# Performance work log

Measured on AMD Instinct MI355X. Metric: run time of the kernel, lower is better.

Reference implementation:

```python
import jax, jax.numpy as jnp
import numpy as np

B, L, N, DOUT = 8, 8192, 256, 256  # batch, seq_len, state_dim, output_dim


def setup_inputs() -> dict:
    key = jax.random.key(0)
    k_u, k_h, k_w = jax.random.split(key, 3)
    u = jax.random.normal(k_u, (B, L, 1), dtype=jnp.float32)
    # impulse response buffer (stands in for A_bar^i @ B_bar rows); decay-scaled for realism
    h = jax.random.normal(k_h, (L, N), dtype=jnp.float32) * 0.02
    W = jax.random.normal(k_w, (DOUT, N), dtype=jnp.float32) * (1.0 / np.sqrt(N))
    return {"u": u, "h": h, "W": W}


def reference(u, h, W):
    L_ = h.shape[0]
    n_fft = 2 * L_
    # FFT-based long convolution: U:[B, n_fft//2+1, 1], H:[n_fft//2+1, N]
    U = jnp.fft.rfft(u, n=n_fft, axis=1)
    H = jnp.fft.rfft(h, n=n_fft, axis=0)
    M = U * H[None, :, :]                      # broadcast channel 1 -> N
    m = jnp.fft.irfft(M, n=n_fft, axis=1)[:, :L_, :]  # [B, L, N]
    return jnp.einsum('bln,on->blo', m, W)     # Linear(state_dim -> output_dim), no bias
```

## Files before the change

kernel.cpp:

```cpp
#include <hip/hip_runtime.h>
#include <hip/hip_bf16.h>
#include <stdint.h>
#include <stddef.h>

typedef __attribute__((ext_vector_type(4))) float f32x4;
typedef __attribute__((ext_vector_type(8))) short s16x8;

#define B_    8
#define L_    8192
#define N_    256
#define DOUT_ 256

__device__ __forceinline__ unsigned short f2bf(float f) {
  unsigned int x = __float_as_uint(f);
  x += 0x7fff + ((x >> 16) & 1);
  return (unsigned short)(x >> 16);
}

__global__ void k_convert(const float* __restrict__ h, const float* __restrict__ W,
                          unsigned short* __restrict__ hb, unsigned short* __restrict__ Wb) {
  int t = blockIdx.x * 256 + threadIdx.x;
  int base = t * 4;
  const int TH = L_ * N_;
  const int TW = DOUT_ * N_;
  if (base < TH) {
    float4 v = *(const float4*)(h + base);
    hb[base + 0] = f2bf(v.x); hb[base + 1] = f2bf(v.y);
    hb[base + 2] = f2bf(v.z); hb[base + 3] = f2bf(v.w);
  } else if (base < TH + TW) {
    int wb = base - TH;
    float4 v = *(const float4*)(W + wb);
    Wb[wb + 0] = f2bf(v.x); Wb[wb + 1] = f2bf(v.y);
    Wb[wb + 2] = f2bf(v.z); Wb[wb + 3] = f2bf(v.w);
  }
}

__global__ void k_amat(const float* __restrict__ u, unsigned short* __restrict__ Am) {
  int t = blockIdx.x * 256 + threadIdx.x;
  int i0 = (t & 15) * 8;
  int lp = (t >> 4) & 127;
  int d  = (t >> 11) & 63;
  int b  = t >> 17;
  const float* ub = u + b * L_;
  int base = 128 * d + lp - i0;
  s16x8 v;
#pragma unroll
  for (int j = 0; j < 8; ++j) {
    int idx = base - j;
    float f = (idx >= 0) ? ub[idx] : 0.0f;
    v[j] = (short)f2bf(f);
  }
  *(s16x8*)(Am + (size_t)t * 8) = v;
}

__global__ void k_gt(const unsigned short* __restrict__ Wb, const unsigned short* __restrict__ hb,
                     unsigned short* __restrict__ gT) {
  int gid  = blockIdx.x * 256 + threadIdx.x;
  int lane = gid & 63;
  int wid  = gid >> 6;
  int o_t  = wid >> 7;
  int i_t  = wid & 127;
  int o0 = o_t * 16, i0 = i_t * 64;
  int ln = lane & 15, hi = lane >> 4;
  f32x4 acc[4] = {};
#pragma unroll
  for (int k0 = 0; k0 < N_; k0 += 32) {
    s16x8 a = *(const s16x8*)(Wb + (o0 + ln) * N_ + k0 + 8 * hi);
#pragma unroll
    for (int ns = 0; ns < 4; ++ns) {
      s16x8 bfr = *(const s16x8*)(hb + (i0 + 16 * ns + ln) * N_ + k0 + 8 * hi);
      acc[ns] = __builtin_amdgcn_mfma_f32_16x16x32_bf16(a, bfr, acc[ns], 0, 0, 0);
    }
  }
#pragma unroll
  for (int ns = 0; ns < 4; ++ns)
#pragma unroll
    for (int q = 0; q < 4; ++q)
      gT[(size_t)(o0 + 4 * hi + q) * L_ + i0 + 16 * ns + ln] = f2bf(acc[ns][q]);
}

__global__ __launch_bounds__(256) void k_main(const unsigned short* __restrict__ Am,
                                              const unsigned short* __restrict__ gT,
                                              float* __restrict__ out) {
  __shared__ short Abuf[128 * 64];
  __shared__ short Bbuf[128 * 64];
  const int c = blockIdx.x;
  const int b = blockIdx.y;
  const int r = 63 - blockIdx.z;
  const int t = threadIdx.x;
  const int lane = t & 63;
  const int w = t >> 6;
  const int wm = (w >> 1) * 64, wn = (w & 1) * 64;
  const int ln = lane & 15, hi = lane >> 4;
  const int ob = c * 128;
  const int trow = t >> 3;
  const int tcol = (t & 7) * 8;
  f32x4 acc[4][4] = {};

  const int nkt = 2 * (r + 1);
  for (int kt = 0; kt < nkt; ++kt) {
    const int i0   = kt * 64;
    const int d    = r - (kt >> 1);
    const int ioff = (kt & 1) * 64;
    const unsigned short* Asrc = Am + (((size_t)(b * 64 + d)) << 14) + ioff + tcol;
    const unsigned short* Bsrc = gT + (size_t)(ob + trow) * L_ + i0 + tcol;
#pragma unroll
    for (int call = 0; call < 4; ++call) {
      __builtin_amdgcn_global_load_lds(
          (const __attribute__((address_space(1))) void*)(Asrc + (size_t)(call * 32 + trow) * 128),
          (__attribute__((address_space(3))) void*)(Abuf + call * 2048 + t * 8),
          16, 0, 0);
    }
#pragma unroll
    for (int call = 0; call < 4; ++call) {
      __builtin_amdgcn_global_load_lds(
          (const __attribute__((address_space(1))) void*)(Bsrc + (size_t)(call * 32) * L_),
          (__attribute__((address_space(3))) void*)(Bbuf + call * 2048 + t * 8),
          16, 0, 0);
    }
    __syncthreads();
#pragma unroll
    for (int k0 = 0; k0 < 64; k0 += 32) {
      s16x8 af[4], bfr[4];
#pragma unroll
      for (int m = 0; m < 4; ++m)
        af[m] = *(const s16x8*)(Abuf + (wm + m * 16 + ln) * 64 + k0 + 8 * hi);
#pragma unroll
      for (int n = 0; n < 4; ++n)
        bfr[n] = *(const s16x8*)(Bbuf + (wn + n * 16 + ln) * 64 + k0 + 8 * hi);
#pragma unroll
      for (int m = 0; m < 4; ++m)
#pragma unroll
        for (int n = 0; n < 4; ++n)
          acc[m][n] = __builtin_amdgcn_mfma_f32_16x16x32_bf16(af[m], bfr[n], acc[m][n], 0, 0, 0);
    }
    __syncthreads();
  }

  const int lb = r * 128;
#pragma unroll
  for (int m = 0; m < 4; ++m)
#pragma unroll
    for (int n = 0; n < 4; ++n)
#pragma unroll
      for (int q = 0; q < 4; ++q) {
        int l = lb + wm + m * 16 + 4 * hi + q;
        int o = ob + wn + n * 16 + ln;
        out[(size_t)(b * L_ + l) * DOUT_ + o] = acc[m][n][q];
      }
}

extern "C" void kernel_launch(void* const* d_in, const int* in_sizes, int n_in,
                              void* d_out, int out_size, void* d_ws, size_t ws_size,
                              hipStream_t stream) {
  const float* u = (const float*)d_in[0];
  const float* h = (const float*)d_in[1];
  const float* W = (const float*)d_in[2];
  float* out = (float*)d_out;

  char* ws = (char*)d_ws;
  unsigned short* hb = (unsigned short*)(ws);
  unsigned short* Wb = (unsigned short*)(ws + (size_t)4 * 1024 * 1024);
  unsigned short* gT = (unsigned short*)(ws + (size_t)4 * 1024 * 1024 + 131072);
  unsigned short* Am = (unsigned short*)(ws + (size_t)8 * 1024 * 1024 + 131072);

  k_convert<<<2112, 256, 0, stream>>>(h, W, hb, Wb);
  k_amat<<<4096, 256, 0, stream>>>(u, Am);
  k_gt<<<512, 256, 0, stream>>>(Wb, hb, gT);
  k_main<<<dim3(2, 8, 64), 256, 0, stream>>>(Am, gT, out);
}
```

Before: 220.4 us.

## Double-buffer main GEMM with 256-row tiles, LDS swizzle and zero block padding

Restructures the main Toeplitz-GEMM kernel to use 512-thread blocks with 256-row output tiles and double-buffered LDS filled by async global-to-LDS loads that overlap the MFMA compute. LDS reads use an XOR swizzle to avoid bank conflicts, and MFMA sections run at raised wave priority. A zero diagonal block (index 64) is added to the A matrix so tiles reaching before the sequence start read zeros instead of branching. hb now aliases the Am workspace region, so k_amat is reordered to run after k_gt. The costs are more LDS per block, fewer total blocks, and extra causal work on the padded zero blocks.

```diff
diff --git a/kernel.cpp b/kernel.cpp
--- a/kernel.cpp
+++ b/kernel.cpp
@@ -39,16 +39,21 @@
   int t = blockIdx.x * 256 + threadIdx.x;
   int i0 = (t & 15) * 8;
   int lp = (t >> 4) & 127;
-  int d  = (t >> 11) & 63;
-  int b  = t >> 17;
-  const float* ub = u + b * L_;
-  int base = 128 * d + lp - i0;
+  int r2 = t >> 11;
+  int d  = r2 % 65;
+  int b  = r2 / 65;
   s16x8 v;
 #pragma unroll
-  for (int j = 0; j < 8; ++j) {
-    int idx = base - j;
-    float f = (idx >= 0) ? ub[idx] : 0.0f;
-    v[j] = (short)f2bf(f);
+  for (int j = 0; j < 8; ++j) v[j] = 0;
+  if (d < 64) {
+    const float* ub = u + b * L_;
+    int base = 128 * d + lp - i0;
+#pragma unroll
+    for (int j = 0; j < 8; ++j) {
+      int idx = base - j;
+      float f = (idx >= 0) ? ub[idx] : 0.0f;
+      v[j] = (short)f2bf(f);
+    }
   }
   *(s16x8*)(Am + (size_t)t * 8) = v;
 }
@@ -79,75 +84,131 @@
       gT[(size_t)(o0 + 4 * hi + q) * L_ + i0 + 16 * ns + ln] = f2bf(acc[ns][q]);
 }
 
-__global__ __launch_bounds__(256) void k_main(const unsigned short* __restrict__ Am,
-                                              const unsigned short* __restrict__ gT,
-                                              float* __restrict__ out) {
-  __shared__ short Abuf[128 * 64];
-  __shared__ short Bbuf[128 * 64];
+__global__ __launch_bounds__(512, 2) void k_main(const unsigned short* __restrict__ Am,
+                                                 const unsigned short* __restrict__ gT,
+                                                 float* __restrict__ out) {
+  __shared__ short As[2][16384];
+  __shared__ short Bs[2][8192];
   const int c = blockIdx.x;
   const int b = blockIdx.y;
-  const int r = 63 - blockIdx.z;
-  const int t = threadIdx.x;
-  const int lane = t & 63;
-  const int w = t >> 6;
-  const int wm = (w >> 1) * 64, wn = (w & 1) * 64;
+  const int R = 31 - blockIdx.z;
+  const int tid = threadIdx.x;
+  const int lane = tid & 63;
+  const int w = tid >> 6;
+  const int wr = w >> 1, wc = w & 1;
   const int ln = lane & 15, hi = lane >> 4;
   const int ob = c * 128;
-  const int trow = t >> 3;
-  const int tcol = (t & 7) * 8;
+
+  const int t3 = tid >> 3;
+  const int sA = ((tid & 7) ^ (t3 & 7)) << 3;
+  const unsigned short* AmB = Am + (size_t)(b * 65) * 16384;
+  const unsigned short* Bb0 = gT + (size_t)(ob + t3) * L_ + sA;
+  const unsigned short* Bb1 = gT + (size_t)(ob + t3 + 64) * L_ + sA;
+  const int rl0 = t3;
+  const int rl1 = 64 + t3;
+
+  const int offA = (wr * 64 + ln) * 64;
+  const int offB = (wc * 64 + ln) * 64;
+  const int sw = ln & 7;
+  const int off_k0 = (hi ^ sw) * 8;
+  const int off_k1 = ((hi + 4) ^ sw) * 8;
+
   f32x4 acc[4][4] = {};
-
-  const int nkt = 2 * (r + 1);
+  const int nkt = 4 * (R + 1);
+
+#define ISSUE_A(ktv, buf) do { \
+    const int kthalf_ = (ktv) >> 1; const int kodd_ = ((ktv) & 1) << 6; \
+    _Pragma("unroll") \
+    for (int q = 0; q < 4; ++q) { \
+      int dd = 2 * R + (q >> 1) - kthalf_; \
+      int sd = dd < 0 ? 64 : dd; \
+      const unsigned short* src = AmB + ((size_t)sd << 14) + ((q & 1 ? rl1 : rl0) << 7) + kodd_ + sA; \
+      __builtin_amdgcn_global_load_lds((const __attribute__((address_space(1))) void*)src, \
+          (__attribute__((address_space(3))) void*)(&As[buf][(tid + 512 * q) * 8]), 16, 0, 0); \
+    } \
+  } while (0)
+
+#define ISSUE_B(ktv, buf) do { \
+    const int kb_ = (ktv) * 64; \
+    __builtin_amdgcn_global_load_lds((const __attribute__((address_space(1))) void*)(Bb0 + kb_), \
+        (__attribute__((address_space(3))) void*)(&Bs[buf][tid * 8]), 16, 0, 0); \
+    __builtin_amdgcn_global_load_lds((const __attribute__((address_space(1))) void*)(Bb1 + kb_), \
+        (__attribute__((address_space(3))) void*)(&Bs[buf][(tid + 512) * 8]), 16, 0, 0); \
+  } while (0)
+
+  ISSUE_A(0, 0);
+  ISSUE_B(0, 0);
+
   for (int kt = 0; kt < nkt; ++kt) {
-    const int i0   = kt * 64;
-    const int d    = r - (kt >> 1);
-    const int ioff = (kt & 1) * 64;
-    const unsigned short* Asrc = Am + (((size_t)(b * 64 + d)) << 14) + ioff + tcol;
-    const unsigned short* Bsrc = gT + (size_t)(ob + trow) * L_ + i0 + tcol;
-#pragma unroll
-    for (int call = 0; call < 4; ++call) {
-      __builtin_amdgcn_global_load_lds(
-          (const __attribute__((address_space(1))) void*)(Asrc + (size_t)(call * 32 + trow) * 128),
-          (__attribute__((address_space(3))) void*)(Abuf + call * 2048 + t * 8),
-          16, 0, 0);
-    }
-#pragma unroll
-    for (int call = 0; call < 4; ++call) {
-      __builtin_amdgcn_global_load_lds(
-          (const __attribute__((address_space(1))) void*)(Bsrc + (size_t)(call * 32) * L_),
-          (__attribute__((address_space(3))) void*)(Bbuf + call * 2048 + t * 8),
-          16, 0, 0);
-    }
-    __syncthreads();
-#pragma unroll
-    for (int k0 = 0; k0 < 64; k0 += 32) {
-      s16x8 af[4], bfr[4];
+    const int cur = kt & 1;
+    const int nxt = cur ^ 1;
+    const int kt1 = (kt + 1 < nkt) ? kt + 1 : kt;
+
+    ISSUE_A(kt1, nxt);
+    asm volatile("s_waitcnt vmcnt(4)" ::: "memory");
+    __builtin_amdgcn_sched_barrier(0);
+    __builtin_amdgcn_s_barrier();
+    __builtin_amdgcn_sched_barrier(0);
+    const short* Ac = &As[cur][0];
+    const short* Bc = &Bs[cur][0];
+    s16x8 af[4][2], bf[2][2];
+#pragma unroll
+    for (int m = 0; m < 4; ++m) {
+      af[m][0] = *(const s16x8*)(Ac + offA + m * 1024 + off_k0);
+      af[m][1] = *(const s16x8*)(Ac + offA + m * 1024 + off_k1);
+    }
+#pragma unroll
+    for (int n = 0; n < 2; ++n) {
+      bf[n][0] = *(const s16x8*)(Bc + offB + n * 1024 + off_k0);
+      bf[n][1] = *(const s16x8*)(Bc + offB + n * 1024 + off_k1);
+    }
+    __builtin_amdgcn_s_setprio(1);
+#pragma unroll
+    for (int kk = 0; kk < 2; ++kk)
 #pragma unroll
       for (int m = 0; m < 4; ++m)
-        af[m] = *(const s16x8*)(Abuf + (wm + m * 16 + ln) * 64 + k0 + 8 * hi);
+#pragma unroll
+        for (int n = 0; n < 2; ++n)
+          acc[m][n] = __builtin_amdgcn_mfma_f32_16x16x32_bf16(af[m][kk], bf[n][kk], acc[m][n], 0, 0, 0);
+    __builtin_amdgcn_s_setprio(0);
+
+    ISSUE_B(kt1, nxt);
+    s16x8 bg[2][2];
+#pragma unroll
+    for (int n = 0; n < 2; ++n) {
+      bg[n][0] = *(const s16x8*)(Bc + offB + (n + 2) * 1024 + off_k0);
+      bg[n][1] = *(const s16x8*)(Bc + offB + (n + 2) * 1024 + off_k1);
+    }
+    __builtin_amdgcn_s_setprio(1);
+#pragma unroll
+    for (int kk = 0; kk < 2; ++kk)
+#pragma unroll
+      for (int m = 0; m < 4; ++m)
+#pragma unroll
+        for (int n = 0; n < 2; ++n)
+          acc[m][n + 2] = __builtin_amdgcn_mfma_f32_16x16x32_bf16(af[m][kk], bg[n][kk], acc[m][n + 2], 0, 0, 0);
+    __builtin_amdgcn_s_setprio(0);
+    __builtin_amdgcn_sched_barrier(0);
+    __builtin_amdgcn_s_barrier();
+    __builtin_amdgcn_sched_barrier(0);
+  }
+
+  asm volatile("s_waitcnt vmcnt(0)" ::: "memory");
+
+  const int l0 = R * 256 + wr * 64 + 4 * hi;
+  const int o0 = ob + wc * 64 + ln;
+  float* outb = out + (size_t)b * L_ * DOUT_;
+#pragma unroll
+  for (int m = 0; m < 4; ++m)
+#pragma unroll
+    for (int q = 0; q < 4; ++q) {
+      float* rowp = outb + (size_t)(l0 + m * 16 + q) * DOUT_ + o0;
 #pragma unroll
       for (int n = 0; n < 4; ++n)
-        bfr[n] = *(const s16x8*)(Bbuf + (wn + n * 16 + ln) * 64 + k0 + 8 * hi);
-#pragma unroll
-      for (int m = 0; m < 4; ++m)
-#pragma unroll
-        for (int n = 0; n < 4; ++n)
-          acc[m][n] = __builtin_amdgcn_mfma_f32_16x16x32_bf16(af[m], bfr[n], acc[m][n], 0, 0, 0);
-    }
-    __syncthreads();
-  }
-
-  const int lb = r * 128;
-#pragma unroll
-  for (int m = 0; m < 4; ++m)
-#pragma unroll
-    for (int n = 0; n < 4; ++n)
-#pragma unroll
-      for (int q = 0; q < 4; ++q) {
-        int l = lb + wm + m * 16 + 4 * hi + q;
-        int o = ob + wn + n * 16 + ln;
-        out[(size_t)(b * L_ + l) * DOUT_ + o] = acc[m][n][q];
-      }
+        rowp[n * 16] = acc[m][n][q];
+    }
+#undef ISSUE_A
+#undef ISSUE_B
 }
 
 extern "C" void kernel_launch(void* const* d_in, const int* in_sizes, int n_in,
@@ -159,13 +220,14 @@
   float* out = (float*)d_out;
 
   char* ws = (char*)d_ws;
-  unsigned short* hb = (unsigned short*)(ws);
-  unsigned short* Wb = (unsigned short*)(ws + (size_t)4 * 1024 * 1024);
-  unsigned short* gT = (unsigned short*)(ws + (size_t)4 * 1024 * 1024 + 131072);
-  unsigned short* Am = (unsigned short*)(ws + (size_t)8 * 1024 * 1024 + 131072);
+  const size_t AM_BYTES = (size_t)8 * 65 * 16384 * 2;
+  unsigned short* Am = (unsigned short*)ws;
+  unsigned short* gT = (unsigned short*)(ws + AM_BYTES);
+  unsigned short* Wb = (unsigned short*)(ws + AM_BYTES + (size_t)4 * 1024 * 1024);
+  unsigned short* hb = (unsigned short*)ws;
 
   k_convert<<<2112, 256, 0, stream>>>(h, W, hb, Wb);
-  k_amat<<<4096, 256, 0, stream>>>(u, Am);
   k_gt<<<512, 256, 0, stream>>>(Wb, hb, gT);
-  k_main<<<dim3(2, 8, 64), 256, 0, stream>>>(Am, gT, out);
-}
+  k_amat<<<4160, 256, 0, stream>>>(u, Am);
+  k_main<<<dim3(2, 8, 32), 512, 0, stream>>>(Am, gT, out);
+}
```

Measured after the change: 201.0 us. 8.8% less time.
